# Optimization experiments

Hardware: AMD Instinct MI355X
Metric: run time of the kernel (lower is better)

## Reference

```python
import jax, jax.numpy as jnp
import numpy as np

D_MODEL = 1024
NUM_HEADS = 16
HEAD_DIM = D_MODEL // NUM_HEADS
MASK_FUTURE = False
NEG_INF = -1.0e9


def setup_inputs() -> dict:
    key = jax.random.key(0)
    ks = jax.random.split(key, 8)
    B, L = 2, 2048
    q = jax.random.normal(ks[0], (B, L, D_MODEL), dtype=jnp.float32)
    k = jax.random.normal(ks[1], (B, L, D_MODEL), dtype=jnp.float32)
    v = jax.random.normal(ks[2], (B, L, D_MODEL), dtype=jnp.float32)
    attention_mask = jnp.ones((B, L), dtype=jnp.int32)
    s = 1.0 / np.sqrt(D_MODEL)
    Wq = jax.random.normal(ks[3], (D_MODEL, D_MODEL), dtype=jnp.float32) * s
    Wk = jax.random.normal(ks[4], (D_MODEL, D_MODEL), dtype=jnp.float32) * s
    Wv = jax.random.normal(ks[5], (D_MODEL, D_MODEL), dtype=jnp.float32) * s
    Wo = jax.random.normal(ks[6], (D_MODEL, D_MODEL), dtype=jnp.float32) * s
    return {"q": q, "k": k, "v": v, "attention_mask": attention_mask,
            "Wq": Wq, "Wk": Wk, "Wv": Wv, "Wo": Wo}


def _split_heads(x):
    B, L, _ = x.shape
    return x.reshape(B, L, NUM_HEADS, HEAD_DIM).transpose(0, 2, 1, 3)  # [B,H,L,Hd]


def reference(q, k, v, attention_mask, Wq, Wk, Wv, Wo):
    B, Lq, _ = q.shape
    Lk = k.shape[1]
    Q = _split_heads(q @ Wq.T)
    K = _split_heads(k @ Wk.T)
    V = _split_heads(v @ Wv.T)
    scale = HEAD_DIM ** 0.5  # per-head D in original Attention
    scores = jnp.einsum('bhqd,bhkd->bhqk', Q, K) / scale
    mask = (attention_mask == 0)[:, None, None, :]  # [B,1,1,Lk]
    scores = jnp.where(mask, NEG_INF, scores)
    if MASK_FUTURE:
        fut = jnp.triu(jnp.ones((Lq, Lk), dtype=bool), k=1)
        scores = jnp.where(fut[None, None], NEG_INF, scores)
    attn = jax.nn.softmax(scores, axis=-1)
    out = jnp.einsum('bhqk,bhkd->bhqd', attn, V)
    out = out.transpose(0, 2, 1, 3).reshape(B, Lq, D_MODEL)
    return out @ Wo.T
```

## Files before the change

kernel.cpp:

```cpp
#include <hip/hip_runtime.h>


#define D_MODEL 1024
#define NH 16
#define HD 64
#define BATCH 2
#define SEQ 2048
#define MROWS (BATCH*SEQ)

typedef unsigned short u16;
typedef __bf16 bf16x8 __attribute__((ext_vector_type(8)));
typedef float f32x4 __attribute__((ext_vector_type(4)));

__device__ __forceinline__ u16 f2bf(float f){
    __bf16 h = (__bf16)f;
    return __builtin_bit_cast(u16, h);
}
__device__ __forceinline__ float fast_exp2(float x){ return __builtin_amdgcn_exp2f(x); }

__device__ __forceinline__ void stage16(const void* g, void* l){
#if __has_builtin(__builtin_amdgcn_global_load_lds)
    __builtin_amdgcn_global_load_lds(
        (__attribute__((address_space(1))) void*)(unsigned long long)(g),
        (__attribute__((address_space(3))) void*)(unsigned int)(unsigned long long)(l),
        16, 0, 0);
#else
    *(uint4*)l = *(const uint4*)g;
#endif
}

__device__ __forceinline__ int detect_f32_block(const u16* q, int tid){
    __shared__ int flag;
    if (tid < 64){
        unsigned e = (q[2*tid]>>7)&0xFFu;
        bool hit = (e>=115u)&&(e<=132u);
        unsigned long long m = __ballot(hit);
        if (tid==0) flag = (__popcll(m) < 32) ? 1 : 0;
    }
    __syncthreads();
    return flag;
}

__global__ __launch_bounds__(256)
void convert_all(const u16* __restrict__ q, const u16* __restrict__ k,
                 const u16* __restrict__ v, const u16* __restrict__ Wq,
                 const u16* __restrict__ Wk, const u16* __restrict__ Wv,
                 const u16* __restrict__ Wo, u16* __restrict__ dst)
{
    int isf32 = detect_f32_block(q, threadIdx.x);
    int bid = blockIdx.x;
    const u16* src; int lb;
    if      (bid < 4096)  { src=q;  lb=bid; }
    else if (bid < 8192)  { src=k;  lb=bid-4096; }
    else if (bid < 12288) { src=v;  lb=bid-8192; }
    else if (bid < 13312) { src=Wq; lb=bid-12288; }
    else if (bid < 14336) { src=Wk; lb=bid-13312; }
    else if (bid < 15360) { src=Wv; lb=bid-14336; }
    else                  { src=Wo; lb=bid-15360; }
    size_t so = (size_t)lb*1024 + threadIdx.x*4;
    size_t dofs = (size_t)bid*1024 + threadIdx.x*4;
    if (isf32){
        float4 x = *(const float4*)((const float*)src + so);
        ushort4 o; o.x=f2bf(x.x); o.y=f2bf(x.y); o.z=f2bf(x.z); o.w=f2bf(x.w);
        *(ushort4*)(dst+dofs) = o;
    } else {
        *(ushort4*)(dst+dofs) = *(const ushort4*)(src+so);
    }
}

__global__ __launch_bounds__(256)
void gemm_qkv(const u16* __restrict__ qb, const u16* __restrict__ kb,
              const u16* __restrict__ vb, const u16* __restrict__ Wqb,
              const u16* __restrict__ Wkb, const u16* __restrict__ Wvb,
              u16* __restrict__ Qh, u16* __restrict__ Kh, u16* __restrict__ Vt)
{
    const int K = 1024;
    __shared__ __align__(16) u16 lA[128*32];
    __shared__ __align__(16) u16 lB[128*32];
    const int z = blockIdx.z;
    const u16* A  = (z==0)? qb  : (z==1)? kb  : vb;
    const u16* Bt = (z==0)? Wqb : (z==1)? Wkb : Wvb;

    const int tid  = threadIdx.x;
    const int wid  = tid>>6, lane = tid&63;
    const int quad = lane>>4, l16 = lane&15;
    const int wm = (wid>>1)*64, wn = (wid&1)*64;
    const int row0 = blockIdx.y*128, col0 = blockIdx.x*128;

    f32x4 acc[4][4];
    #pragma unroll
    for (int i=0;i<4;i++)
        #pragma unroll
        for (int j=0;j<4;j++) acc[i][j] = (f32x4){0.f,0.f,0.f,0.f};

    for (int k0=0; k0<K; k0+=32){
        #pragma unroll
        for (int s=0;s<2;s++){
            int c = tid + s*256;
            int r = c>>2, cc = (c&3)*8;
            stage16(&A [(size_t)(row0+r)*K + k0 + cc], &lA[c*8]);
            stage16(&Bt[(size_t)(col0+r)*K + k0 + cc], &lB[c*8]);
        }
        __syncthreads();
        bf16x8 af[4], bfr[4];
        #pragma unroll
        for (int mi=0;mi<4;mi++) af[mi]  = *(const bf16x8*)&lA[(wm+mi*16+l16)*32 + quad*8];
        #pragma unroll
        for (int ni=0;ni<4;ni++) bfr[ni] = *(const bf16x8*)&lB[(wn+ni*16+l16)*32 + quad*8];
        #pragma unroll
        for (int mi=0;mi<4;mi++)
            #pragma unroll
            for (int ni=0;ni<4;ni++)
                acc[mi][ni] = __builtin_amdgcn_mfma_f32_16x16x32_bf16(af[mi], bfr[ni], acc[mi][ni], 0,0,0);
        __syncthreads();
    }

    u16* Csh = (z==0)? Qh : Kh;
    #pragma unroll
    for (int mi=0;mi<4;mi++){
        #pragma unroll
        for (int ni=0;ni<4;ni++){
            int col = col0 + wn + ni*16 + l16;
            #pragma unroll
            for (int r=0;r<4;r++){
                int row = row0 + wm + mi*16 + quad*4 + r;
                u16 o = f2bf(acc[mi][ni][r]);
                int b = row>>11, i = row&2047, h = col>>6, d = col&63;
                if (z<2) Csh[((((size_t)(b*NH+h))*SEQ + i)<<6) + d] = o;
                else     Vt[((size_t)((b*NH+h)*HD + d))*SEQ + i] = o;
            }
        }
    }
}

__global__ __launch_bounds__(256)
void gemm_out(const u16* __restrict__ A, const u16* __restrict__ Bt,
              void* __restrict__ Cv, const u16* __restrict__ qref)
{
    const int K = 1024, N = 1024;
    int outf32 = detect_f32_block(qref, threadIdx.x);
    __shared__ __align__(16) u16 lA[64*32];
    __shared__ __align__(16) u16 lB[128*32];
    const int tid  = threadIdx.x;
    const int wid  = tid>>6, lane = tid&63;
    const int quad = lane>>4, l16 = lane&15;
    const int wm = (wid>>1)*32, wn = (wid&1)*64;
    const int row0 = blockIdx.y*64, col0 = blockIdx.x*128;

    f32x4 acc[2][4];
    #pragma unroll
    for (int i=0;i<2;i++)
        #pragma unroll
        for (int j=0;j<4;j++) acc[i][j] = (f32x4){0.f,0.f,0.f,0.f};

    for (int k0=0; k0<K; k0+=32){
        {
            int r = tid>>2, cc = (tid&3)*8;
            stage16(&A[(size_t)(row0+r)*K + k0 + cc], &lA[tid*8]);
        }
        #pragma unroll
        for (int s=0;s<2;s++){
            int c = tid + s*256;
            int r = c>>2, cc = (c&3)*8;
            stage16(&Bt[(size_t)(col0+r)*K + k0 + cc], &lB[c*8]);
        }
        __syncthreads();
        bf16x8 af[2], bfr[4];
        #pragma unroll
        for (int mi=0;mi<2;mi++) af[mi]  = *(const bf16x8*)&lA[(wm+mi*16+l16)*32 + quad*8];
        #pragma unroll
        for (int ni=0;ni<4;ni++) bfr[ni] = *(const bf16x8*)&lB[(wn+ni*16+l16)*32 + quad*8];
        #pragma unroll
        for (int mi=0;mi<2;mi++)
            #pragma unroll
            for (int ni=0;ni<4;ni++)
                acc[mi][ni] = __builtin_amdgcn_mfma_f32_16x16x32_bf16(af[mi], bfr[ni], acc[mi][ni], 0,0,0);
        __syncthreads();
    }

    #pragma unroll
    for (int mi=0;mi<2;mi++){
        #pragma unroll
        for (int ni=0;ni<4;ni++){
            int col = col0 + wn + ni*16 + l16;
            #pragma unroll
            for (int r=0;r<4;r++){
                int row = row0 + wm + mi*16 + quad*4 + r;
                float f = acc[mi][ni][r];
                if (outf32) ((float*)Cv)[(size_t)row*N + col] = f;
                else        ((u16*)Cv)[(size_t)row*N + col] = f2bf(f);
            }
        }
    }
}

#define KVT 4096
#define SW(row, c8) ((row)*64 + ((((c8) ^ ((row)&7)))*8))

__global__ __launch_bounds__(256)
void attn3(const u16* __restrict__ Qh, const u16* __restrict__ Kh,
           const u16* __restrict__ Vt, const int* __restrict__ mask,
           u16* __restrict__ ctx)
{
    __shared__ __align__(16) u16 lk[2*KVT];
    __shared__ __align__(16) u16 lv[2*KVT];
    __shared__ __align__(16) u16 lps[128*64];
    __shared__ unsigned mb[64];

    const int id = blockIdx.x;
    const int bh = (id&7)*4 + (id>>7);
    const int qb = (id>>3)&15;
    const int b = bh>>4, h = bh&15;
    const int i0 = qb*128;
    const int tid = threadIdx.x;
    const int wv = tid>>6, lane = tid&63;
    const int quad = lane>>4, l16 = lane&15;

    const u16* Qp  = Qh + ((size_t)bh*SEQ + i0)*HD;
    const u16* Kp  = Kh + (size_t)bh*SEQ*HD;
    const u16* Vtp = Vt + (size_t)bh*HD*SEQ;
    const int* mp  = mask + b*SEQ;

    #pragma unroll
    for (int s=0;s<4;s++){
        int c = tid + s*256;
        int r = c>>3, c8 = c&7;
        *(uint4*)&lps[SW(r,c8)] = *(const uint4*)&Qp[(size_t)r*HD + c8*8];
    }
    if (tid < 64){
        unsigned w = 0;
        #pragma unroll 8
        for (int i=0;i<32;i++) w |= (mp[tid*32+i] ? 1u:0u) << i;
        mb[tid] = w;
    }
    #pragma unroll
    for (int s=0;s<2;s++){
        int c = tid + s*256;
        int r = c>>3, c8 = c&7;
        *(uint4*)&lk[SW(r,c8)] = *(const uint4*)&Kp[(size_t)r*HD + c8*8];
        *(uint4*)&lv[SW(r,c8)] = *(const uint4*)&Vtp[(size_t)r*SEQ + c8*8];
    }
    __syncthreads();

    bf16x8 aq[2][2];
    #pragma unroll
    for (int mi=0;mi<2;mi++)
        #pragma unroll
        for (int kk=0;kk<2;kk++)
            aq[mi][kk] = *(const bf16x8*)&lps[SW(wv*32+mi*16+l16, kk*4+quad)];

    const int prow0 = wv*32;

    u16 onebits[8] = {0x3F80,0x3F80,0x3F80,0x3F80,0x3F80,0x3F80,0x3F80,0x3F80};
    bf16x8 bones = *(bf16x8*)onebits;

    f32x4 Oacc[2][4];
    f32x4 Lacc[2];
    #pragma unroll
    for (int mi=0;mi<2;mi++){
        Lacc[mi] = (f32x4){0.f,0.f,0.f,0.f};
        #pragma unroll
        for (int dn=0;dn<4;dn++) Oacc[mi][dn] = (f32x4){0.f,0.f,0.f,0.f};
    }

    const float SC = 0.125f * 1.44269504f;

    for (int t=0; t<32; t++){
        const int j0 = t*64;
        const u16* lkc = lk + (t&1)*KVT;
        const u16* lvc = lv + (t&1)*KVT;
        u16* lkn = lk + ((t&1)^1)*KVT;
        u16* lvn = lv + ((t&1)^1)*KVT;

        __syncthreads();

        uint4 gk[2], gv[2];
        if (t < 31){
            #pragma unroll
            for (int s=0;s<2;s++){
                int c = tid + s*256;
                int r = c>>3, c8 = c&7;
                gk[s] = *(const uint4*)&Kp[(size_t)(j0+64+r)*HD + c8*8];
                gv[s] = *(const uint4*)&Vtp[(size_t)r*SEQ + j0+64 + c8*8];
            }
        }

        f32x4 sfr[2][4];
        #pragma unroll
        for (int jn=0;jn<4;jn++){
            bf16x8 bk0 = *(const bf16x8*)&lkc[SW(jn*16+l16, quad)];
            bf16x8 bk1 = *(const bf16x8*)&lkc[SW(jn*16+l16, 4+quad)];
            #pragma unroll
            for (int mi=0;mi<2;mi++){
                f32x4 a0 = (f32x4){0.f,0.f,0.f,0.f};
                a0 = __builtin_amdgcn_mfma_f32_16x16x32_bf16(aq[mi][0], bk0, a0, 0,0,0);
                a0 = __builtin_amdgcn_mfma_f32_16x16x32_bf16(aq[mi][1], bk1, a0, 0,0,0);
                sfr[mi][jn] = a0;
            }
        }

        unsigned mw0 = mb[t*2], mw1 = mb[t*2+1];
        #pragma unroll
        for (int jn=0;jn<4;jn++){
            unsigned mw = (jn<2)? mw0 : mw1;
            int sh = (jn&1)*16 + l16;
            float bias = ((mw>>sh)&1u) ? 0.f : -1.5e9f;
            int c8 = jn*2 + (l16>>3), cb = l16&7;
            #pragma unroll
            for (int mi=0;mi<2;mi++){
                #pragma unroll
                for (int r=0;r<4;r++){
                    float p = fast_exp2(sfr[mi][jn][r]*SC + bias);
                    lps[SW(prow0+mi*16+quad*4+r, c8) + cb] = f2bf(p);
                }
            }
        }
        bf16x8 ap[2][2];
        #pragma unroll
        for (int mi=0;mi<2;mi++)
            #pragma unroll
            for (int kk=0;kk<2;kk++)
                ap[mi][kk] = *(const bf16x8*)&lps[SW(prow0+mi*16+l16, kk*4+quad)];

        #pragma unroll
        for (int dn=0;dn<4;dn++){
            #pragma unroll
            for (int kk=0;kk<2;kk++){
                bf16x8 bv = *(const bf16x8*)&lvc[SW(dn*16+l16, kk*4+quad)];
                #pragma unroll
                for (int mi=0;mi<2;mi++)
                    Oacc[mi][dn] = __builtin_amdgcn_mfma_f32_16x16x32_bf16(ap[mi][kk], bv, Oacc[mi][dn], 0,0,0);
            }
        }
        #pragma unroll
        for (int mi=0;mi<2;mi++)
            #pragma unroll
            for (int kk=0;kk<2;kk++)
                Lacc[mi] = __builtin_amdgcn_mfma_f32_16x16x32_bf16(ap[mi][kk], bones, Lacc[mi], 0,0,0);

        if (t < 31){
            #pragma unroll
            for (int s=0;s<2;s++){
                int c = tid + s*256;
                int r = c>>3, c8 = c&7;
                *(uint4*)&lkn[SW(r,c8)] = gk[s];
                *(uint4*)&lvn[SW(r,c8)] = gv[s];
            }
        }
    }

    #pragma unroll
    for (int mi=0;mi<2;mi++){
        f32x4 rl;
        #pragma unroll
        for (int r=0;r<4;r++) rl[r] = 1.0f / Lacc[mi][r];
        #pragma unroll
        for (int dn=0;dn<4;dn++){
            int col = h*HD + dn*16 + l16;
            #pragma unroll
            for (int r=0;r<4;r++){
                int i = i0 + wv*32 + mi*16 + quad*4 + r;
                ctx[((size_t)(b*SEQ + i))*D_MODEL + col] = f2bf(Oacc[mi][dn][r]*rl[r]);
            }
        }
    }
}

extern "C" void kernel_launch(void* const* d_in, const int* in_sizes, int n_in,
                              void* d_out, int out_size, void* d_ws, size_t ws_size,
                              hipStream_t stream)
{
    (void)in_sizes; (void)n_in; (void)out_size; (void)ws_size;
    const u16* q    = (const u16*)d_in[0];
    const u16* k    = (const u16*)d_in[1];
    const u16* v    = (const u16*)d_in[2];
    const int* mask = (const int*)d_in[3];
    const u16* Wq   = (const u16*)d_in[4];
    const u16* Wk   = (const u16*)d_in[5];
    const u16* Wv   = (const u16*)d_in[6];
    const u16* Wo   = (const u16*)d_in[7];

    const size_t TEN = (size_t)MROWS * D_MODEL;
    const size_t WEL = (size_t)D_MODEL * D_MODEL;
    u16* qb  = (u16*)d_ws;
    u16* kb  = qb + TEN;
    u16* vb  = kb + TEN;
    u16* Wqb = vb + TEN;
    u16* Wkb = Wqb + WEL;
    u16* Wvb = Wkb + WEL;
    u16* Wob = Wvb + WEL;
    u16* Qh  = Wob + WEL;
    u16* Kh  = Qh + TEN;
    u16* Vtr = Kh + TEN;
    u16* ctx = Vtr + TEN;

    dim3 bb(256);
    convert_all<<<dim3(16384), bb, 0, stream>>>(q,k,v,Wq,Wk,Wv,Wo, qb);
    gemm_qkv<<<dim3(8,32,3), bb, 0, stream>>>(qb,kb,vb, Wqb,Wkb,Wvb, Qh,Kh,Vtr);
    attn3<<<dim3(512), bb, 0, stream>>>(Qh, Kh, Vtr, mask, ctx);
    gemm_out<<<dim3(8,64), bb, 0, stream>>>(ctx, Wob, d_out, q);
}
```

Before: 241.8 us.

## Fuse fp32-to-bf16 conversion into GEMM staging and widen attention blocks

Removes the separate convert_all kernel and instead converts fp32 inputs and weights to bf16 while staging tiles into LDS inside the QKV and output GEMMs. This avoids a full write and re-read of converted copies. The cost is that the fp32 path now uses register loads instead of direct global-to-LDS loads. Separately, the attention kernel goes from 256 to 512 threads per block, with each wave handling 16 query rows instead of 32. That halves per-wave registers and cooperative load work, but halves K/V reuse per wave.

```diff
diff --git a/kernel.cpp b/kernel.cpp
--- a/kernel.cpp
+++ b/kernel.cpp
@@ -41,45 +41,33 @@
     return flag;
 }
 
+__device__ __forceinline__ void stage_cvt(const void* srcv, size_t eoff, u16* lds, int isf32){
+    if (isf32){
+        const float* s = (const float*)srcv + eoff;
+        float4 a0 = *(const float4*)s;
+        float4 a1 = *(const float4*)(s+4);
+        ushort4 o0; o0.x=f2bf(a0.x); o0.y=f2bf(a0.y); o0.z=f2bf(a0.z); o0.w=f2bf(a0.w);
+        ushort4 o1; o1.x=f2bf(a1.x); o1.y=f2bf(a1.y); o1.z=f2bf(a1.z); o1.w=f2bf(a1.w);
+        *(ushort4*)lds = o0; *(ushort4*)(lds+4) = o1;
+    } else {
+        stage16((const u16*)srcv + eoff, lds);
+    }
+}
+
 __global__ __launch_bounds__(256)
-void convert_all(const u16* __restrict__ q, const u16* __restrict__ k,
-                 const u16* __restrict__ v, const u16* __restrict__ Wq,
-                 const u16* __restrict__ Wk, const u16* __restrict__ Wv,
-                 const u16* __restrict__ Wo, u16* __restrict__ dst)
-{
-    int isf32 = detect_f32_block(q, threadIdx.x);
-    int bid = blockIdx.x;
-    const u16* src; int lb;
-    if      (bid < 4096)  { src=q;  lb=bid; }
-    else if (bid < 8192)  { src=k;  lb=bid-4096; }
-    else if (bid < 12288) { src=v;  lb=bid-8192; }
-    else if (bid < 13312) { src=Wq; lb=bid-12288; }
-    else if (bid < 14336) { src=Wk; lb=bid-13312; }
-    else if (bid < 15360) { src=Wv; lb=bid-14336; }
-    else                  { src=Wo; lb=bid-15360; }
-    size_t so = (size_t)lb*1024 + threadIdx.x*4;
-    size_t dofs = (size_t)bid*1024 + threadIdx.x*4;
-    if (isf32){
-        float4 x = *(const float4*)((const float*)src + so);
-        ushort4 o; o.x=f2bf(x.x); o.y=f2bf(x.y); o.z=f2bf(x.z); o.w=f2bf(x.w);
-        *(ushort4*)(dst+dofs) = o;
-    } else {
-        *(ushort4*)(dst+dofs) = *(const ushort4*)(src+so);
-    }
-}
-
-__global__ __launch_bounds__(256)
-void gemm_qkv(const u16* __restrict__ qb, const u16* __restrict__ kb,
-              const u16* __restrict__ vb, const u16* __restrict__ Wqb,
-              const u16* __restrict__ Wkb, const u16* __restrict__ Wvb,
-              u16* __restrict__ Qh, u16* __restrict__ Kh, u16* __restrict__ Vt)
+void gemm_qkv(const void* __restrict__ qv, const void* __restrict__ kv,
+              const void* __restrict__ vv, const void* __restrict__ Wqv,
+              const void* __restrict__ Wkv, const void* __restrict__ Wvv,
+              u16* __restrict__ Qh, u16* __restrict__ Kh, u16* __restrict__ Vt,
+              const u16* __restrict__ qref)
 {
     const int K = 1024;
+    int isf32 = detect_f32_block(qref, threadIdx.x);
     __shared__ __align__(16) u16 lA[128*32];
     __shared__ __align__(16) u16 lB[128*32];
     const int z = blockIdx.z;
-    const u16* A  = (z==0)? qb  : (z==1)? kb  : vb;
-    const u16* Bt = (z==0)? Wqb : (z==1)? Wkb : Wvb;
+    const void* A  = (z==0)? qv  : (z==1)? kv  : vv;
+    const void* Bt = (z==0)? Wqv : (z==1)? Wkv : Wvv;
 
     const int tid  = threadIdx.x;
     const int wid  = tid>>6, lane = tid&63;
@@ -98,8 +86,8 @@
         for (int s=0;s<2;s++){
             int c = tid + s*256;
             int r = c>>2, cc = (c&3)*8;
-            stage16(&A [(size_t)(row0+r)*K + k0 + cc], &lA[c*8]);
-            stage16(&Bt[(size_t)(col0+r)*K + k0 + cc], &lB[c*8]);
+            stage_cvt(A,  (size_t)(row0+r)*K + k0 + cc, &lA[c*8], isf32);
+            stage_cvt(Bt, (size_t)(col0+r)*K + k0 + cc, &lB[c*8], isf32);
         }
         __syncthreads();
         bf16x8 af[4], bfr[4];
@@ -134,11 +122,11 @@
 }
 
 __global__ __launch_bounds__(256)
-void gemm_out(const u16* __restrict__ A, const u16* __restrict__ Bt,
+void gemm_out(const u16* __restrict__ A, const void* __restrict__ Bt,
               void* __restrict__ Cv, const u16* __restrict__ qref)
 {
     const int K = 1024, N = 1024;
-    int outf32 = detect_f32_block(qref, threadIdx.x);
+    int isf32 = detect_f32_block(qref, threadIdx.x);
     __shared__ __align__(16) u16 lA[64*32];
     __shared__ __align__(16) u16 lB[128*32];
     const int tid  = threadIdx.x;
@@ -162,7 +150,7 @@
         for (int s=0;s<2;s++){
             int c = tid + s*256;
             int r = c>>2, cc = (c&3)*8;
-            stage16(&Bt[(size_t)(col0+r)*K + k0 + cc], &lB[c*8]);
+            stage_cvt(Bt, (size_t)(col0+r)*K + k0 + cc, &lB[c*8], isf32);
         }
         __syncthreads();
         bf16x8 af[2], bfr[4];
@@ -187,8 +175,8 @@
             for (int r=0;r<4;r++){
                 int row = row0 + wm + mi*16 + quad*4 + r;
                 float f = acc[mi][ni][r];
-                if (outf32) ((float*)Cv)[(size_t)row*N + col] = f;
-                else        ((u16*)Cv)[(size_t)row*N + col] = f2bf(f);
+                if (isf32) ((float*)Cv)[(size_t)row*N + col] = f;
+                else       ((u16*)Cv)[(size_t)row*N + col] = f2bf(f);
             }
         }
     }
@@ -197,8 +185,8 @@
 #define KVT 4096
 #define SW(row, c8) ((row)*64 + ((((c8) ^ ((row)&7)))*8))
 
-__global__ __launch_bounds__(256)
-void attn3(const u16* __restrict__ Qh, const u16* __restrict__ Kh,
+__global__ __launch_bounds__(512, 4)
+void attn4(const u16* __restrict__ Qh, const u16* __restrict__ Kh,
            const u16* __restrict__ Vt, const int* __restrict__ mask,
            u16* __restrict__ ctx)
 {
@@ -222,8 +210,8 @@
     const int* mp  = mask + b*SEQ;
 
     #pragma unroll
-    for (int s=0;s<4;s++){
-        int c = tid + s*256;
+    for (int s=0;s<2;s++){
+        int c = tid + s*512;
         int r = c>>3, c8 = c&7;
         *(uint4*)&lps[SW(r,c8)] = *(const uint4*)&Qp[(size_t)r*HD + c8*8];
     }
@@ -233,35 +221,27 @@
         for (int i=0;i<32;i++) w |= (mp[tid*32+i] ? 1u:0u) << i;
         mb[tid] = w;
     }
-    #pragma unroll
-    for (int s=0;s<2;s++){
-        int c = tid + s*256;
-        int r = c>>3, c8 = c&7;
+    {
+        int r = tid>>3, c8 = tid&7;
         *(uint4*)&lk[SW(r,c8)] = *(const uint4*)&Kp[(size_t)r*HD + c8*8];
         *(uint4*)&lv[SW(r,c8)] = *(const uint4*)&Vtp[(size_t)r*SEQ + c8*8];
     }
     __syncthreads();
 
-    bf16x8 aq[2][2];
-    #pragma unroll
-    for (int mi=0;mi<2;mi++)
-        #pragma unroll
-        for (int kk=0;kk<2;kk++)
-            aq[mi][kk] = *(const bf16x8*)&lps[SW(wv*32+mi*16+l16, kk*4+quad)];
-
-    const int prow0 = wv*32;
+    bf16x8 aq[2];
+    #pragma unroll
+    for (int kk=0;kk<2;kk++)
+        aq[kk] = *(const bf16x8*)&lps[SW(wv*16+l16, kk*4+quad)];
+
+    const int prow0 = wv*16;
 
     u16 onebits[8] = {0x3F80,0x3F80,0x3F80,0x3F80,0x3F80,0x3F80,0x3F80,0x3F80};
     bf16x8 bones = *(bf16x8*)onebits;
 
-    f32x4 Oacc[2][4];
-    f32x4 Lacc[2];
-    #pragma unroll
-    for (int mi=0;mi<2;mi++){
-        Lacc[mi] = (f32x4){0.f,0.f,0.f,0.f};
-        #pragma unroll
-        for (int dn=0;dn<4;dn++) Oacc[mi][dn] = (f32x4){0.f,0.f,0.f,0.f};
-    }
+    f32x4 Oacc[4];
+    f32x4 Lacc = (f32x4){0.f,0.f,0.f,0.f};
+    #pragma unroll
+    for (int dn=0;dn<4;dn++) Oacc[dn] = (f32x4){0.f,0.f,0.f,0.f};
 
     const float SC = 0.125f * 1.44269504f;
 
@@ -274,29 +254,22 @@
 
         __syncthreads();
 
-        uint4 gk[2], gv[2];
+        uint4 gk, gv;
         if (t < 31){
-            #pragma unroll
-            for (int s=0;s<2;s++){
-                int c = tid + s*256;
-                int r = c>>3, c8 = c&7;
-                gk[s] = *(const uint4*)&Kp[(size_t)(j0+64+r)*HD + c8*8];
-                gv[s] = *(const uint4*)&Vtp[(size_t)r*SEQ + j0+64 + c8*8];
-            }
-        }
-
-        f32x4 sfr[2][4];
+            int r = tid>>3, c8 = tid&7;
+            gk = *(const uint4*)&Kp[(size_t)(j0+64+r)*HD + c8*8];
+            gv = *(const uint4*)&Vtp[(size_t)r*SEQ + j0+64 + c8*8];
+        }
+
+        f32x4 sfr[4];
         #pragma unroll
         for (int jn=0;jn<4;jn++){
             bf16x8 bk0 = *(const bf16x8*)&lkc[SW(jn*16+l16, quad)];
             bf16x8 bk1 = *(const bf16x8*)&lkc[SW(jn*16+l16, 4+quad)];
-            #pragma unroll
-            for (int mi=0;mi<2;mi++){
-                f32x4 a0 = (f32x4){0.f,0.f,0.f,0.f};
-                a0 = __builtin_amdgcn_mfma_f32_16x16x32_bf16(aq[mi][0], bk0, a0, 0,0,0);
-                a0 = __builtin_amdgcn_mfma_f32_16x16x32_bf16(aq[mi][1], bk1, a0, 0,0,0);
-                sfr[mi][jn] = a0;
-            }
+            f32x4 a0 = (f32x4){0.f,0.f,0.f,0.f};
+            a0 = __builtin_amdgcn_mfma_f32_16x16x32_bf16(aq[0], bk0, a0, 0,0,0);
+            a0 = __builtin_amdgcn_mfma_f32_16x16x32_bf16(aq[1], bk1, a0, 0,0,0);
+            sfr[jn] = a0;
         }
 
         unsigned mw0 = mb[t*2], mw1 = mb[t*2+1];
@@ -307,61 +280,45 @@
             float bias = ((mw>>sh)&1u) ? 0.f : -1.5e9f;
             int c8 = jn*2 + (l16>>3), cb = l16&7;
             #pragma unroll
-            for (int mi=0;mi<2;mi++){
-                #pragma unroll
-                for (int r=0;r<4;r++){
-                    float p = fast_exp2(sfr[mi][jn][r]*SC + bias);
-                    lps[SW(prow0+mi*16+quad*4+r, c8) + cb] = f2bf(p);
-                }
+            for (int r=0;r<4;r++){
+                float p = fast_exp2(sfr[jn][r]*SC + bias);
+                lps[SW(prow0+quad*4+r, c8) + cb] = f2bf(p);
             }
         }
-        bf16x8 ap[2][2];
-        #pragma unroll
-        for (int mi=0;mi<2;mi++)
-            #pragma unroll
-            for (int kk=0;kk<2;kk++)
-                ap[mi][kk] = *(const bf16x8*)&lps[SW(prow0+mi*16+l16, kk*4+quad)];
+        bf16x8 ap[2];
+        #pragma unroll
+        for (int kk=0;kk<2;kk++)
+            ap[kk] = *(const bf16x8*)&lps[SW(prow0+l16, kk*4+quad)];
 
         #pragma unroll
         for (int dn=0;dn<4;dn++){
             #pragma unroll
             for (int kk=0;kk<2;kk++){
                 bf16x8 bv = *(const bf16x8*)&lvc[SW(dn*16+l16, kk*4+quad)];
-                #pragma unroll
-                for (int mi=0;mi<2;mi++)
-                    Oacc[mi][dn] = __builtin_amdgcn_mfma_f32_16x16x32_bf16(ap[mi][kk], bv, Oacc[mi][dn], 0,0,0);
+                Oacc[dn] = __builtin_amdgcn_mfma_f32_16x16x32_bf16(ap[kk], bv, Oacc[dn], 0,0,0);
             }
         }
         #pragma unroll
-        for (int mi=0;mi<2;mi++)
-            #pragma unroll
-            for (int kk=0;kk<2;kk++)
-                Lacc[mi] = __builtin_amdgcn_mfma_f32_16x16x32_bf16(ap[mi][kk], bones, Lacc[mi], 0,0,0);
+        for (int kk=0;kk<2;kk++)
+            Lacc = __builtin_amdgcn_mfma_f32_16x16x32_bf16(ap[kk], bones, Lacc, 0,0,0);
 
         if (t < 31){
-            #pragma unroll
-            for (int s=0;s<2;s++){
-                int c = tid + s*256;
-                int r = c>>3, c8 = c&7;
-                *(uint4*)&lkn[SW(r,c8)] = gk[s];
-                *(uint4*)&lvn[SW(r,c8)] = gv[s];
-            }
-        }
-    }
-
-    #pragma unroll
-    for (int mi=0;mi<2;mi++){
-        f32x4 rl;
-        #pragma unroll
-        for (int r=0;r<4;r++) rl[r] = 1.0f / Lacc[mi][r];
-        #pragma unroll
-        for (int dn=0;dn<4;dn++){
-            int col = h*HD + dn*16 + l16;
-            #pragma unroll
-            for (int r=0;r<4;r++){
-                int i = i0 + wv*32 + mi*16 + quad*4 + r;
-                ctx[((size_t)(b*SEQ + i))*D_MODEL + col] = f2bf(Oacc[mi][dn][r]*rl[r]);
-            }
+            int r = tid>>3, c8 = tid&7;
+            *(uint4*)&lkn[SW(r,c8)] = gk;
+            *(uint4*)&lvn[SW(r,c8)] = gv;
+        }
+    }
+
+    f32x4 rl;
+    #pragma unroll
+    for (int r=0;r<4;r++) rl[r] = 1.0f / Lacc[r];
+    #pragma unroll
+    for (int dn=0;dn<4;dn++){
+        int col = h*HD + dn*16 + l16;
+        #pragma unroll
+        for (int r=0;r<4;r++){
+            int i = i0 + wv*16 + quad*4 + r;
+            ctx[((size_t)(b*SEQ + i))*D_MODEL + col] = f2bf(Oacc[dn][r]*rl[r]);
         }
     }
 }
@@ -371,32 +328,23 @@
                               hipStream_t stream)
 {
     (void)in_sizes; (void)n_in; (void)out_size; (void)ws_size;
-    const u16* q    = (const u16*)d_in[0];
-    const u16* k    = (const u16*)d_in[1];
-    const u16* v    = (const u16*)d_in[2];
-    const int* mask = (const int*)d_in[3];
-    const u16* Wq   = (const u16*)d_in[4];
-    const u16* Wk   = (const u16*)d_in[5];
-    const u16* Wv   = (const u16*)d_in[6];
-    const u16* Wo   = (const u16*)d_in[7];
+    const void* q    = d_in[0];
+    const void* k    = d_in[1];
+    const void* v    = d_in[2];
+    const int* mask  = (const int*)d_in[3];
+    const void* Wq   = d_in[4];
+    const void* Wk   = d_in[5];
+    const void* Wv   = d_in[6];
+    const void* Wo   = d_in[7];
+    const u16* qref  = (const u16*)d_in[0];
 
     const size_t TEN = (size_t)MROWS * D_MODEL;
-    const size_t WEL = (size_t)D_MODEL * D_MODEL;
-    u16* qb  = (u16*)d_ws;
-    u16* kb  = qb + TEN;
-    u16* vb  = kb + TEN;
-    u16* Wqb = vb + TEN;
-    u16* Wkb = Wqb + WEL;
-    u16* Wvb = Wkb + WEL;
-    u16* Wob = Wvb + WEL;
-    u16* Qh  = Wob + WEL;
+    u16* Qh  = (u16*)d_ws;
     u16* Kh  = Qh + TEN;
     u16* Vtr = Kh + TEN;
     u16* ctx = Vtr + TEN;
 
-    dim3 bb(256);
-    convert_all<<<dim3(16384), bb, 0, stream>>>(q,k,v,Wq,Wk,Wv,Wo, qb);
-    gemm_qkv<<<dim3(8,32,3), bb, 0, stream>>>(qb,kb,vb, Wqb,Wkb,Wvb, Qh,Kh,Vtr);
-    attn3<<<dim3(512), bb, 0, stream>>>(Qh, Kh, Vtr, mask, ctx);
-    gemm_out<<<dim3(8,64), bb, 0, stream>>>(ctx, Wob, d_out, q);
-}
+    gemm_qkv<<<dim3(8,32,3), dim3(256), 0, stream>>>(q,k,v, Wq,Wk,Wv, Qh,Kh,Vtr, qref);
+    attn4<<<dim3(512), dim3(512), 0, stream>>>(Qh, Kh, Vtr, mask, ctx);
+    gemm_out<<<dim3(8,64), dim3(256), 0, stream>>>(ctx, Wo, d_out, qref);
+}
```

New measurement: 292.8 us. +21.1%, slower.

## Split attention KV range across two wave groups and merge partial results

Applied to the files above, without the earlier changes.

The attention kernel now runs 512 threads per block: two groups of four waves each process half of the key/value sequence for the same 128 query rows. Each group uses its own LDS K/V buffer, which replaces the previous double-buffering. The groups' partial output accumulators and row sums are combined through LDS at the end. The aim is more waves per query tile, and so more latency hiding, at the cost of losing the old buffer overlap, adding an extra barrier per iteration, and a reduction epilogue.

```diff
diff --git a/kernel.cpp b/kernel.cpp
--- a/kernel.cpp
+++ b/kernel.cpp
@@ -197,14 +197,15 @@
 #define KVT 4096
 #define SW(row, c8) ((row)*64 + ((((c8) ^ ((row)&7)))*8))
 
-__global__ __launch_bounds__(256)
-void attn3(const u16* __restrict__ Qh, const u16* __restrict__ Kh,
+__global__ __launch_bounds__(512, 4)
+void attn5(const u16* __restrict__ Qh, const u16* __restrict__ Kh,
            const u16* __restrict__ Vt, const int* __restrict__ mask,
            u16* __restrict__ ctx)
 {
     __shared__ __align__(16) u16 lk[2*KVT];
     __shared__ __align__(16) u16 lv[2*KVT];
-    __shared__ __align__(16) u16 lps[128*64];
+    __shared__ __align__(16) u16 lps[256*64];
+    __shared__ float lO[128];
     __shared__ unsigned mb[64];
 
     const int id = blockIdx.x;
@@ -214,6 +215,7 @@
     const int i0 = qb*128;
     const int tid = threadIdx.x;
     const int wv = tid>>6, lane = tid&63;
+    const int g = wv>>2, w4 = wv&3;
     const int quad = lane>>4, l16 = lane&15;
 
     const u16* Qp  = Qh + ((size_t)bh*SEQ + i0)*HD;
@@ -221,9 +223,19 @@
     const u16* Vtp = Vt + (size_t)bh*HD*SEQ;
     const int* mp  = mask + b*SEQ;
 
-    #pragma unroll
-    for (int s=0;s<4;s++){
-        int c = tid + s*256;
+    uint4 gk[2], gv[2];
+    #pragma unroll
+    for (int s=0;s<2;s++){
+        int c = tid + s*512;
+        int gg = c>>9, l = c&511, r = l>>3, c8 = l&7;
+        int j0g = gg*1024;
+        gk[s] = *(const uint4*)&Kp[(size_t)(j0g + r)*HD + c8*8];
+        gv[s] = *(const uint4*)&Vtp[(size_t)r*SEQ + j0g + c8*8];
+    }
+
+    #pragma unroll
+    for (int s=0;s<2;s++){
+        int c = tid + s*512;
         int r = c>>3, c8 = c&7;
         *(uint4*)&lps[SW(r,c8)] = *(const uint4*)&Qp[(size_t)r*HD + c8*8];
     }
@@ -233,13 +245,6 @@
         for (int i=0;i<32;i++) w |= (mp[tid*32+i] ? 1u:0u) << i;
         mb[tid] = w;
     }
-    #pragma unroll
-    for (int s=0;s<2;s++){
-        int c = tid + s*256;
-        int r = c>>3, c8 = c&7;
-        *(uint4*)&lk[SW(r,c8)] = *(const uint4*)&Kp[(size_t)r*HD + c8*8];
-        *(uint4*)&lv[SW(r,c8)] = *(const uint4*)&Vtp[(size_t)r*SEQ + c8*8];
-    }
     __syncthreads();
 
     bf16x8 aq[2][2];
@@ -247,8 +252,11 @@
     for (int mi=0;mi<2;mi++)
         #pragma unroll
         for (int kk=0;kk<2;kk++)
-            aq[mi][kk] = *(const bf16x8*)&lps[SW(wv*32+mi*16+l16, kk*4+quad)];
-
+            aq[mi][kk] = *(const bf16x8*)&lps[SW(w4*32+mi*16+l16, kk*4+quad)];
+    __syncthreads();
+
+    const u16* lkc = lk + g*KVT;
+    const u16* lvc = lv + g*KVT;
     const int prow0 = wv*32;
 
     u16 onebits[8] = {0x3F80,0x3F80,0x3F80,0x3F80,0x3F80,0x3F80,0x3F80,0x3F80};
@@ -265,23 +273,24 @@
 
     const float SC = 0.125f * 1.44269504f;
 
-    for (int t=0; t<32; t++){
-        const int j0 = t*64;
-        const u16* lkc = lk + (t&1)*KVT;
-        const u16* lvc = lv + (t&1)*KVT;
-        u16* lkn = lk + ((t&1)^1)*KVT;
-        u16* lvn = lv + ((t&1)^1)*KVT;
-
-        __syncthreads();
-
-        uint4 gk[2], gv[2];
-        if (t < 31){
+    for (int t=0; t<16; t++){
+        #pragma unroll
+        for (int s=0;s<2;s++){
+            int c = tid + s*512;
+            int gg = c>>9, l = c&511, r = l>>3, c8 = l&7;
+            *(uint4*)&lk[gg*KVT + SW(r,c8)] = gk[s];
+            *(uint4*)&lv[gg*KVT + SW(r,c8)] = gv[s];
+        }
+        __syncthreads();
+
+        if (t < 15){
             #pragma unroll
             for (int s=0;s<2;s++){
-                int c = tid + s*256;
-                int r = c>>3, c8 = c&7;
-                gk[s] = *(const uint4*)&Kp[(size_t)(j0+64+r)*HD + c8*8];
-                gv[s] = *(const uint4*)&Vtp[(size_t)r*SEQ + j0+64 + c8*8];
+                int c = tid + s*512;
+                int gg = c>>9, l = c&511, r = l>>3, c8 = l&7;
+                int j0g = gg*1024 + (t+1)*64;
+                gk[s] = *(const uint4*)&Kp[(size_t)(j0g + r)*HD + c8*8];
+                gv[s] = *(const uint4*)&Vtp[(size_t)r*SEQ + j0g + c8*8];
             }
         }
 
@@ -299,7 +308,8 @@
             }
         }
 
-        unsigned mw0 = mb[t*2], mw1 = mb[t*2+1];
+        int tg = g*16 + t;
+        unsigned mw0 = mb[tg*2], mw1 = mb[tg*2+1];
         #pragma unroll
         for (int jn=0;jn<4;jn++){
             unsigned mw = (jn<2)? mw0 : mw1;
@@ -338,29 +348,45 @@
             for (int kk=0;kk<2;kk++)
                 Lacc[mi] = __builtin_amdgcn_mfma_f32_16x16x32_bf16(ap[mi][kk], bones, Lacc[mi], 0,0,0);
 
-        if (t < 31){
-            #pragma unroll
-            for (int s=0;s<2;s++){
-                int c = tid + s*256;
-                int r = c>>3, c8 = c&7;
-                *(uint4*)&lkn[SW(r,c8)] = gk[s];
-                *(uint4*)&lvn[SW(r,c8)] = gv[s];
-            }
-        }
-    }
-
-    #pragma unroll
-    for (int mi=0;mi<2;mi++){
-        f32x4 rl;
-        #pragma unroll
-        for (int r=0;r<4;r++) rl[r] = 1.0f / Lacc[mi][r];
-        #pragma unroll
-        for (int dn=0;dn<4;dn++){
-            int col = h*HD + dn*16 + l16;
+        __syncthreads();
+    }
+
+    float* lpf = (float*)lps;
+    if (g==1){
+        #pragma unroll
+        for (int mi=0;mi<2;mi++){
+            #pragma unroll
+            for (int dn=0;dn<4;dn++){
+                #pragma unroll
+                for (int r=0;r<4;r++)
+                    lpf[(w4*32+mi*16+quad*4+r)*64 + dn*16+l16] = Oacc[mi][dn][r];
+            }
+            if (l16==0){
+                #pragma unroll
+                for (int r=0;r<4;r++) lO[w4*32+mi*16+quad*4+r] = Lacc[mi][r];
+            }
+        }
+    }
+    __syncthreads();
+    if (g==0){
+        #pragma unroll
+        for (int mi=0;mi<2;mi++){
+            f32x4 rl;
             #pragma unroll
             for (int r=0;r<4;r++){
-                int i = i0 + wv*32 + mi*16 + quad*4 + r;
-                ctx[((size_t)(b*SEQ + i))*D_MODEL + col] = f2bf(Oacc[mi][dn][r]*rl[r]);
+                int row = w4*32+mi*16+quad*4+r;
+                rl[r] = 1.0f / (Lacc[mi][r] + lO[row]);
+            }
+            #pragma unroll
+            for (int dn=0;dn<4;dn++){
+                int col = h*HD + dn*16 + l16;
+                #pragma unroll
+                for (int r=0;r<4;r++){
+                    int row = w4*32+mi*16+quad*4+r;
+                    float o = Oacc[mi][dn][r] + lpf[row*64 + dn*16+l16];
+                    int i = i0 + row;
+                    ctx[((size_t)(b*SEQ + i))*D_MODEL + col] = f2bf(o*rl[r]);
+                }
             }
         }
     }
@@ -394,9 +420,8 @@
     u16* Vtr = Kh + TEN;
     u16* ctx = Vtr + TEN;
 
-    dim3 bb(256);
-    convert_all<<<dim3(16384), bb, 0, stream>>>(q,k,v,Wq,Wk,Wv,Wo, qb);
-    gemm_qkv<<<dim3(8,32,3), bb, 0, stream>>>(qb,kb,vb, Wqb,Wkb,Wvb, Qh,Kh,Vtr);
-    attn3<<<dim3(512), bb, 0, stream>>>(Qh, Kh, Vtr, mask, ctx);
-    gemm_out<<<dim3(8,64), bb, 0, stream>>>(ctx, Wob, d_out, q);
-}
+    convert_all<<<dim3(16384), dim3(256), 0, stream>>>(q,k,v,Wq,Wk,Wv,Wo, qb);
+    gemm_qkv<<<dim3(8,32,3), dim3(256), 0, stream>>>(qb,kb,vb, Wqb,Wkb,Wvb, Qh,Kh,Vtr);
+    attn5<<<dim3(512), dim3(512), 0, stream>>>(Qh, Kh, Vtr, mask, ctx);
+    gemm_out<<<dim3(8,64), dim3(256), 0, stream>>>(ctx, Wob, d_out, q);
+}
```

Result: slower. 363.1 us (+50.2%).

## Keep attention probabilities in registers using transposed QK^T and 16x16x16 MFMA

Applied to the files above, without the earlier changes.

Computes the score tile transposed by swapping the MFMA operands (K as A, Q as B). Each lane then holds exactly the probability elements it needs as the A operand of 16x16x16 bf16 MFMAs for the PV product and the row-sum. This removes the round trip of writing P to shared memory and reading it back. The cost is twice as many smaller-K MFMA instructions for PV and L, plus narrower 8-byte V loads from LDS.

```diff
diff --git a/kernel.cpp b/kernel.cpp
--- a/kernel.cpp
+++ b/kernel.cpp
@@ -11,6 +11,11 @@
 typedef unsigned short u16;
 typedef __bf16 bf16x8 __attribute__((ext_vector_type(8)));
 typedef float f32x4 __attribute__((ext_vector_type(4)));
+
+#if __has_builtin(__builtin_amdgcn_mfma_f32_16x16x16bf16_1k)
+#define HAVE_M16 1
+typedef short s16x4 __attribute__((ext_vector_type(4)));
+#endif
 
 __device__ __forceinline__ u16 f2bf(float f){
     __bf16 h = (__bf16)f;
@@ -197,8 +202,9 @@
 #define KVT 4096
 #define SW(row, c8) ((row)*64 + ((((c8) ^ ((row)&7)))*8))
 
+#ifdef HAVE_M16
 __global__ __launch_bounds__(256)
-void attn3(const u16* __restrict__ Qh, const u16* __restrict__ Kh,
+void attn6(const u16* __restrict__ Qh, const u16* __restrict__ Kh,
            const u16* __restrict__ Vt, const int* __restrict__ mask,
            u16* __restrict__ ctx)
 {
@@ -249,10 +255,7 @@
         for (int kk=0;kk<2;kk++)
             aq[mi][kk] = *(const bf16x8*)&lps[SW(wv*32+mi*16+l16, kk*4+quad)];
 
-    const int prow0 = wv*32;
-
-    u16 onebits[8] = {0x3F80,0x3F80,0x3F80,0x3F80,0x3F80,0x3F80,0x3F80,0x3F80};
-    bf16x8 bones = *(bf16x8*)onebits;
+    s16x4 bones4 = {0x3F80, 0x3F80, 0x3F80, 0x3F80};
 
     f32x4 Oacc[2][4];
     f32x4 Lacc[2];
@@ -285,6 +288,171 @@
             }
         }
 
+        f32x4 sfr[4][2];
+        #pragma unroll
+        for (int jn=0;jn<4;jn++){
+            bf16x8 bk0 = *(const bf16x8*)&lkc[SW(jn*16+l16, quad)];
+            bf16x8 bk1 = *(const bf16x8*)&lkc[SW(jn*16+l16, 4+quad)];
+            #pragma unroll
+            for (int mi=0;mi<2;mi++){
+                f32x4 a0 = (f32x4){0.f,0.f,0.f,0.f};
+                a0 = __builtin_amdgcn_mfma_f32_16x16x32_bf16(bk0, aq[mi][0], a0, 0,0,0);
+                a0 = __builtin_amdgcn_mfma_f32_16x16x32_bf16(bk1, aq[mi][1], a0, 0,0,0);
+                sfr[jn][mi] = a0;
+            }
+        }
+
+        unsigned mw0 = mb[t*2], mw1 = mb[t*2+1];
+        s16x4 ap16[2][4];
+        #pragma unroll
+        for (int jn=0;jn<4;jn++){
+            unsigned mw = (jn<2)? mw0 : mw1;
+            unsigned nib = (mw >> (((jn&1)<<4) + quad*4)) & 0xFu;
+            #pragma unroll
+            for (int mi=0;mi<2;mi++){
+                #pragma unroll
+                for (int r=0;r<4;r++){
+                    float bias = ((nib>>r)&1u) ? 0.f : -1.5e9f;
+                    float p = fast_exp2(sfr[jn][mi][r]*SC + bias);
+                    ap16[mi][jn][r] = (short)f2bf(p);
+                }
+            }
+        }
+
+        #pragma unroll
+        for (int kks=0;kks<4;kks++){
+            #pragma unroll
+            for (int dn=0;dn<4;dn++){
+                int c8 = kks*2 + (quad>>1);
+                s16x4 bv = *(const s16x4*)&lvc[SW(dn*16+l16, c8) + (quad&1)*4];
+                #pragma unroll
+                for (int mi=0;mi<2;mi++)
+                    Oacc[mi][dn] = __builtin_amdgcn_mfma_f32_16x16x16bf16_1k(
+                        ap16[mi][kks], bv, Oacc[mi][dn], 0,0,0);
+            }
+            #pragma unroll
+            for (int mi=0;mi<2;mi++)
+                Lacc[mi] = __builtin_amdgcn_mfma_f32_16x16x16bf16_1k(
+                    ap16[mi][kks], bones4, Lacc[mi], 0,0,0);
+        }
+
+        if (t < 31){
+            #pragma unroll
+            for (int s=0;s<2;s++){
+                int c = tid + s*256;
+                int r = c>>3, c8 = c&7;
+                *(uint4*)&lkn[SW(r,c8)] = gk[s];
+                *(uint4*)&lvn[SW(r,c8)] = gv[s];
+            }
+        }
+    }
+
+    #pragma unroll
+    for (int mi=0;mi<2;mi++){
+        f32x4 rl;
+        #pragma unroll
+        for (int r=0;r<4;r++) rl[r] = 1.0f / Lacc[mi][r];
+        #pragma unroll
+        for (int dn=0;dn<4;dn++){
+            int col = h*HD + dn*16 + l16;
+            #pragma unroll
+            for (int r=0;r<4;r++){
+                int i = i0 + wv*32 + mi*16 + quad*4 + r;
+                ctx[((size_t)(b*SEQ + i))*D_MODEL + col] = f2bf(Oacc[mi][dn][r]*rl[r]);
+            }
+        }
+    }
+}
+
+#else
+
+__global__ __launch_bounds__(256)
+void attn6(const u16* __restrict__ Qh, const u16* __restrict__ Kh,
+           const u16* __restrict__ Vt, const int* __restrict__ mask,
+           u16* __restrict__ ctx)
+{
+    __shared__ __align__(16) u16 lk[2*KVT];
+    __shared__ __align__(16) u16 lv[2*KVT];
+    __shared__ __align__(16) u16 lps[128*64];
+    __shared__ unsigned mb[64];
+
+    const int id = blockIdx.x;
+    const int bh = (id&7)*4 + (id>>7);
+    const int qb = (id>>3)&15;
+    const int b = bh>>4, h = bh&15;
+    const int i0 = qb*128;
+    const int tid = threadIdx.x;
+    const int wv = tid>>6, lane = tid&63;
+    const int quad = lane>>4, l16 = lane&15;
+
+    const u16* Qp  = Qh + ((size_t)bh*SEQ + i0)*HD;
+    const u16* Kp  = Kh + (size_t)bh*SEQ*HD;
+    const u16* Vtp = Vt + (size_t)bh*HD*SEQ;
+    const int* mp  = mask + b*SEQ;
+
+    #pragma unroll
+    for (int s=0;s<4;s++){
+        int c = tid + s*256;
+        int r = c>>3, c8 = c&7;
+        *(uint4*)&lps[SW(r,c8)] = *(const uint4*)&Qp[(size_t)r*HD + c8*8];
+    }
+    if (tid < 64){
+        unsigned w = 0;
+        #pragma unroll 8
+        for (int i=0;i<32;i++) w |= (mp[tid*32+i] ? 1u:0u) << i;
+        mb[tid] = w;
+    }
+    #pragma unroll
+    for (int s=0;s<2;s++){
+        int c = tid + s*256;
+        int r = c>>3, c8 = c&7;
+        *(uint4*)&lk[SW(r,c8)] = *(const uint4*)&Kp[(size_t)r*HD + c8*8];
+        *(uint4*)&lv[SW(r,c8)] = *(const uint4*)&Vtp[(size_t)r*SEQ + c8*8];
+    }
+    __syncthreads();
+
+    bf16x8 aq[2][2];
+    #pragma unroll
+    for (int mi=0;mi<2;mi++)
+        #pragma unroll
+        for (int kk=0;kk<2;kk++)
+            aq[mi][kk] = *(const bf16x8*)&lps[SW(wv*32+mi*16+l16, kk*4+quad)];
+
+    const int prow0 = wv*32;
+    u16 onebits[8] = {0x3F80,0x3F80,0x3F80,0x3F80,0x3F80,0x3F80,0x3F80,0x3F80};
+    bf16x8 bones = *(bf16x8*)onebits;
+
+    f32x4 Oacc[2][4];
+    f32x4 Lacc[2];
+    #pragma unroll
+    for (int mi=0;mi<2;mi++){
+        Lacc[mi] = (f32x4){0.f,0.f,0.f,0.f};
+        #pragma unroll
+        for (int dn=0;dn<4;dn++) Oacc[mi][dn] = (f32x4){0.f,0.f,0.f,0.f};
+    }
+
+    const float SC = 0.125f * 1.44269504f;
+
+    for (int t=0; t<32; t++){
+        const int j0 = t*64;
+        const u16* lkc = lk + (t&1)*KVT;
+        const u16* lvc = lv + (t&1)*KVT;
+        u16* lkn = lk + ((t&1)^1)*KVT;
+        u16* lvn = lv + ((t&1)^1)*KVT;
+
+        __syncthreads();
+
+        uint4 gk[2], gv[2];
+        if (t < 31){
+            #pragma unroll
+            for (int s=0;s<2;s++){
+                int c = tid + s*256;
+                int r = c>>3, c8 = c&7;
+                gk[s] = *(const uint4*)&Kp[(size_t)(j0+64+r)*HD + c8*8];
+                gv[s] = *(const uint4*)&Vtp[(size_t)r*SEQ + j0+64 + c8*8];
+            }
+        }
+
         f32x4 sfr[2][4];
         #pragma unroll
         for (int jn=0;jn<4;jn++){
@@ -365,6 +533,7 @@
         }
     }
 }
+#endif
 
 extern "C" void kernel_launch(void* const* d_in, const int* in_sizes, int n_in,
                               void* d_out, int out_size, void* d_ws, size_t ws_size,
@@ -394,9 +563,8 @@
     u16* Vtr = Kh + TEN;
     u16* ctx = Vtr + TEN;
 
-    dim3 bb(256);
-    convert_all<<<dim3(16384), bb, 0, stream>>>(q,k,v,Wq,Wk,Wv,Wo, qb);
-    gemm_qkv<<<dim3(8,32,3), bb, 0, stream>>>(qb,kb,vb, Wqb,Wkb,Wvb, Qh,Kh,Vtr);
-    attn3<<<dim3(512), bb, 0, stream>>>(Qh, Kh, Vtr, mask, ctx);
-    gemm_out<<<dim3(8,64), bb, 0, stream>>>(ctx, Wob, d_out, q);
-}
+    convert_all<<<dim3(16384), dim3(256), 0, stream>>>(q,k,v,Wq,Wk,Wv,Wo, qb);
+    gemm_qkv<<<dim3(8,32,3), dim3(256), 0, stream>>>(qb,kb,vb, Wqb,Wkb,Wvb, Qh,Kh,Vtr);
+    attn6<<<dim3(512), dim3(256), 0, stream>>>(Qh, Kh, Vtr, mask, ctx);
+    gemm_out<<<dim3(8,64), dim3(256), 0, stream>>>(ctx, Wob, d_out, q);
+}
```

New measurement: 255.1 us. 1.05x slower.
